# Performance work log

Measured on AMD Instinct MI355X. Metric: run time of the kernel, lower is better.

## Reference

```python
import jax, jax.numpy as jnp
import numpy as np

EMBED_DIM = 1024
B, T = 8, 2048


def setup_inputs() -> dict:
    key = jax.random.key(0)
    kx, kw, kb = jax.random.split(key, 3)
    x = jax.random.normal(kx, (B, T, EMBED_DIM), dtype=jnp.float32)
    # nn.Linear(embed_dim, 3*embed_dim): weight [3E, E], bias [3E]
    bound = 1.0 / np.sqrt(EMBED_DIM)
    W = jax.random.uniform(kw, (3 * EMBED_DIM, EMBED_DIM), minval=-bound, maxval=bound, dtype=jnp.float32)
    b = jax.random.uniform(kb, (3 * EMBED_DIM,), minval=-bound, maxval=bound, dtype=jnp.float32)
    return {"x": x, "W": W, "b": b}


def reference(x, W, b):
    E = x.shape[-1]
    qkv = jnp.einsum('bte,fe->btf', x, W) + b            # [B,T,3E]
    q, k, v = jnp.split(qkv, 3, axis=-1)                 # each [B,T,E]
    scale = 1.0 / jnp.sqrt(jnp.asarray(E, dtype=x.dtype))
    scores = jnp.einsum('bqe,bke->bqk', q, k) * scale    # [B,T,T]
    Tq = x.shape[1]
    causal = jnp.tril(jnp.ones((Tq, Tq), dtype=bool))
    scores = jnp.where(causal[None, :, :], scores, jnp.asarray(-jnp.inf, dtype=x.dtype))
    attn = jax.nn.softmax(scores, axis=-1)
    y = jnp.einsum('bqk,bke->bqe', attn, v)              # [B,T,E]
    return y
```

## Files before the change

### kernel.cpp

```cpp
#include <hip/hip_runtime.h>

typedef unsigned short u16;
typedef unsigned int u32;
typedef __attribute__((ext_vector_type(4))) float f32x4;
typedef __attribute__((ext_vector_type(8))) short bf16x8;

#define T_DIM 2048
#define E_DIM 1024
#define NBATCH 8
#define BK 32
#define BUFP 24576
#define COREP_LDS (3 * BUFP)

struct alignas(8)  U16x4 { u16 x, y, z, w; };
struct alignas(16) F32x4 { float x, y, z, w; };

__device__ __forceinline__ u16 f2bf(float f) {
  u32 u = __float_as_uint(f);
  u += 0x7FFFu + ((u >> 16) & 1u);
  return (u16)(u >> 16);
}

__device__ __forceinline__ void gld16(u16* lds, const u16* g) {
  __builtin_amdgcn_global_load_lds((const __attribute__((address_space(1))) void*)g,
                                   (__attribute__((address_space(3))) void*)lds, 16, 0, 0);
}

__device__ __forceinline__ u32 swz7(u32 x) { return x ^ (((x >> 7) & 7u) << 4); }

__device__ __forceinline__ int xcd_swz(int orig, int nwg) {
  int q = nwg >> 3, r = nwg & 7;
  int x = orig & 7, l = orig >> 3;
  return (x < r ? x * (q + 1) : r * (q + 1) + (x - r) * q) + l;
}

#define LGKM0_PIN() do { asm volatile("s_waitcnt lgkmcnt(0)" ::: "memory"); \
                         __builtin_amdgcn_sched_barrier(0); } while (0)

__device__ __forceinline__ void gemm128n(const u16* __restrict__ A, const u16* __restrict__ B,
                                         int lda, int ldb, int nK, char* lds0, f32x4 acc[4][4])
{
  const int tid = threadIdx.x, lane = tid & 63, wave = tid >> 6;
  const int wr = wave >> 2, wc = wave & 3;

  const u16* sA0; const u16* sBp[2];
  {
    u32 g = swz7((u32)tid * 16u);
    sA0 = A + (size_t)(g >> 6) * lda + ((g & 63u) >> 1);
  }
#pragma unroll
  for (int c = 0; c < 2; ++c) {
    u32 g = swz7((u32)(c * 8192 + tid * 16));
    sBp[c] = B + (size_t)(g >> 6) * ldb + ((g & 63u) >> 1);
  }
  const u32 doff = (u32)tid * 16u;

  auto stageA = [&](char* buf, int t) {
    gld16((u16*)(buf + doff), sA0 + t * BK);
  };
  auto stageB = [&](char* buf, int t) {
#pragma unroll
    for (int c = 0; c < 2; ++c)
      gld16((u16*)(buf + 8192 + c * 8192 + doff), sBp[c] + t * BK);
  };

  const u32 cb = (u32)(lane >> 4) * 16u;
  u32 aoff[4], boff[4];
#pragma unroll
  for (int m = 0; m < 4; ++m)
    aoff[m] = swz7((u32)(wr * 64 + m * 16 + (lane & 15)) * 64u + cb);
#pragma unroll
  for (int n = 0; n < 4; ++n)
    boff[n] = 8192u + swz7((u32)(wc * 64 + n * 16 + (lane & 15)) * 64u + cb);

  stageA(lds0, 0); stageB(lds0, 0);
  stageA(lds0 + BUFP, 1); stageB(lds0 + BUFP, 1);

  int bc = 0;
  bf16x8 a[2], b[4];
  for (int t = 0; t < nK; ++t) {
    char* bufR = lds0 + bc * BUFP;
    int b2 = bc + 2; if (b2 >= 3) b2 -= 3;
    char* bufW = lds0 + b2 * BUFP;

    if (t + 1 < nK) asm volatile("s_waitcnt vmcnt(3)" ::: "memory");
    else            asm volatile("s_waitcnt vmcnt(0)" ::: "memory");
    __builtin_amdgcn_s_barrier();
    __builtin_amdgcn_sched_barrier(0);

    if (t + 2 < nK) stageA(bufW, t + 2);
    a[0] = *(const bf16x8*)(bufR + aoff[0]);
    a[1] = *(const bf16x8*)(bufR + aoff[1]);
#pragma unroll
    for (int n = 0; n < 4; ++n) b[n] = *(const bf16x8*)(bufR + boff[n]);
    LGKM0_PIN();
    __builtin_amdgcn_s_setprio(1);
#pragma unroll
    for (int j = 0; j < 2; ++j)
#pragma unroll
      for (int n = 0; n < 4; ++n)
        acc[j][n] = __builtin_amdgcn_mfma_f32_16x16x32_bf16(a[j], b[n], acc[j][n], 0, 0, 0);
    __builtin_amdgcn_s_setprio(0);
    __builtin_amdgcn_sched_barrier(0);

    if (t + 2 < nK) stageB(bufW, t + 2);
    a[0] = *(const bf16x8*)(bufR + aoff[2]);
    a[1] = *(const bf16x8*)(bufR + aoff[3]);
    LGKM0_PIN();
    __builtin_amdgcn_s_setprio(1);
#pragma unroll
    for (int j = 0; j < 2; ++j)
#pragma unroll
      for (int n = 0; n < 4; ++n)
        acc[2 + j][n] = __builtin_amdgcn_mfma_f32_16x16x32_bf16(a[j], b[n], acc[2 + j][n], 0, 0, 0);
    __builtin_amdgcn_s_setprio(0);
    __builtin_amdgcn_sched_barrier(0);

    bc = bc + 1 == 3 ? 0 : bc + 1;
  }
}

__global__ __launch_bounds__(256) void k_cvt(const float* __restrict__ in, u16* __restrict__ out, int n4)
{
  int i = blockIdx.x * 256 + threadIdx.x;
  if (i >= n4) return;
  F32x4 v = *(const F32x4*)&in[(size_t)i * 4];
  U16x4 o;
  o.x = f2bf(v.x); o.y = f2bf(v.y); o.z = f2bf(v.z); o.w = f2bf(v.w);
  *(U16x4*)&out[(size_t)i * 4] = o;
}

__global__ __launch_bounds__(512, 4) void k_qkv(const u16* __restrict__ Xb, const u16* __restrict__ Wb,
                                                const float* __restrict__ bias,
                                                u16* __restrict__ Q, u16* __restrict__ Kmat,
                                                u16* __restrict__ Vt)
{
  __shared__ __align__(16) char lds[COREP_LDS];
  const int wg = xcd_swz(blockIdx.x, gridDim.x);
  const int my = wg / 12, nx = wg % 12;
  const int m0 = my * 128, n0 = nx * 256;
  const int tid = threadIdx.x, lane = tid & 63, wave = tid >> 6;
  const int wr = wave >> 2, wc = wave & 3;
  f32x4 acc[4][4] = {};
  gemm128n(Xb + (size_t)m0 * E_DIM, Wb + (size_t)n0 * E_DIM, E_DIM, E_DIM, E_DIM / BK, lds, acc);
  __syncthreads();

  char* wsl = lds + wave * 8192;
  const int region = nx >> 2;
  const int nlb = (n0 & (E_DIM - 1)) + wc * 64;
  const int g4 = (lane >> 4) << 2;

  if (region < 2) {
    u16* dst = region ? Kmat : Q;
#pragma unroll
    for (int n = 0; n < 4; ++n) {
      const float bn = bias[n0 + wc * 64 + n * 16 + (lane & 15)];
#pragma unroll
      for (int m = 0; m < 4; ++m)
#pragma unroll
        for (int r = 0; r < 4; ++r) {
          const int rl = m * 16 + g4 + r;
          const int cl = n * 16 + (lane & 15);
          u32 byte = (u32)(rl * 128 + cl * 2) ^ (u32)((rl & 7) << 4);
          *(u16*)(wsl + byte) = f2bf(acc[m][n][r] + bn);
        }
    }
    asm volatile("s_waitcnt lgkmcnt(0)" ::: "memory");
    const int rowb = m0 + wr * 64;
#pragma unroll
    for (int it = 0; it < 8; ++it) {
      const int rl = it * 8 + (lane >> 3);
      const int c16 = lane & 7;
      u32 byte = (u32)(rl * 128 + c16 * 16) ^ (u32)((rl & 7) << 4);
      bf16x8 v = *(const bf16x8*)(wsl + byte);
      *(bf16x8*)&dst[(size_t)(rowb + rl) * E_DIM + nlb + c16 * 8] = v;
    }
  } else {
    const int bl = m0 >> 11;
    const int tb = (m0 & (T_DIM - 1)) + wr * 64;
#pragma unroll
    for (int n = 0; n < 4; ++n) {
      const float bn = bias[n0 + wc * 64 + n * 16 + (lane & 15)];
      const int e_l = n * 16 + (lane & 15);
#pragma unroll
      for (int m = 0; m < 4; ++m)
#pragma unroll
        for (int r = 0; r < 4; ++r) {
          const int tl = m * 16 + g4 + r;
          u32 byte = (u32)(e_l * 128 + tl * 2) ^ (u32)((e_l & 7) << 4);
          *(u16*)(wsl + byte) = f2bf(acc[m][n][r] + bn);
        }
    }
    asm volatile("s_waitcnt lgkmcnt(0)" ::: "memory");
#pragma unroll
    for (int it = 0; it < 8; ++it) {
      const int e_l = it * 8 + (lane >> 3);
      const int t16 = lane & 7;
      u32 byte = (u32)(e_l * 128 + t16 * 16) ^ (u32)((e_l & 7) << 4);
      bf16x8 v = *(const bf16x8*)(wsl + byte);
      *(bf16x8*)&Vt[((size_t)bl * E_DIM + nlb + e_l) * T_DIM + tb + t16 * 8] = v;
    }
  }
}

__global__ __launch_bounds__(512, 4) void k_sp(const u16* __restrict__ Q, const u16* __restrict__ Kmat,
                                               u16* __restrict__ P, float* __restrict__ lc)
{
  __shared__ __align__(16) char lds[COREP_LDS];
  const int wg = xcd_swz(blockIdx.x, gridDim.x);
  const int b = wg / 72;
  int ti = wg % 72;
  int iq = 0;
  while (ti >= (iq >> 1) + 1) { ti -= (iq >> 1) + 1; ++iq; }
  const int ik = ti;
  const int tid = threadIdx.x, lane = tid & 63, wave = tid >> 6;
  const int wr = wave >> 2, wc = wave & 3;
  const int g4 = (lane >> 4) << 2;
  f32x4 acc[4][4] = {};
  const u16* Qp = Q    + (size_t)b * T_DIM * E_DIM + (size_t)iq * 128 * E_DIM;
  const u16* Kp = Kmat + (size_t)b * T_DIM * E_DIM + (size_t)ik * 256 * E_DIM;
  gemm128n(Qp, Kp, E_DIM, E_DIM, E_DIM / BK, lds, acc);
  __syncthreads();

  const float scale = 0.03125f;
  const bool diag = (ik == (iq >> 1));
  const int diagoff = iq * 128 - ik * 256;
#pragma unroll
  for (int n = 0; n < 4; ++n) {
    const int cl = wc * 64 + n * 16 + (lane & 15);
#pragma unroll
    for (int m = 0; m < 4; ++m) {
      const int rl0 = wr * 64 + m * 16 + g4;
#pragma unroll
      for (int r = 0; r < 4; ++r) {
        if (diag && cl > diagoff + rl0 + r) acc[m][n][r] = 0.f;
        else acc[m][n][r] = __expf(fminf(acc[m][n][r] * scale, 60.f));
      }
    }
  }

  float* red2 = (float*)lds;
  float Ls[4][4];
#pragma unroll
  for (int m = 0; m < 4; ++m)
#pragma unroll
    for (int r = 0; r < 4; ++r) {
      float s = acc[m][0][r] + acc[m][1][r] + acc[m][2][r] + acc[m][3][r];
#pragma unroll
      for (int off = 1; off <= 8; off <<= 1) s += __shfl_xor(s, off, 64);
      Ls[m][r] = s;
    }
  if ((lane & 15) == 0) {
#pragma unroll
    for (int m = 0; m < 4; ++m)
#pragma unroll
      for (int r = 0; r < 4; ++r)
        red2[wc * 128 + wr * 64 + m * 16 + g4 + r] = Ls[m][r];
  }
  __syncthreads();
  if (wc == 0 && (lane & 15) == 0) {
#pragma unroll
    for (int m = 0; m < 4; ++m)
#pragma unroll
      for (int r = 0; r < 4; ++r) {
        const int row = wr * 64 + m * 16 + g4 + r;
        const float l = red2[row] + red2[128 + row] + red2[256 + row] + red2[384 + row];
        lc[((size_t)b * T_DIM + iq * 128 + row) * 8 + ik] = l;
      }
  }
  __syncthreads();

  u16* Pb = P + (size_t)b * T_DIM * T_DIM;
  char* wsl = lds + wave * 8192;
#pragma unroll
  for (int n = 0; n < 4; ++n)
#pragma unroll
    for (int m = 0; m < 4; ++m)
#pragma unroll
      for (int r = 0; r < 4; ++r) {
        const int rl = m * 16 + g4 + r;
        const int cl = n * 16 + (lane & 15);
        u32 byte = (u32)(rl * 128 + cl * 2) ^ (u32)((rl & 7) << 4);
        *(u16*)(wsl + byte) = f2bf(acc[m][n][r]);
      }
  asm volatile("s_waitcnt lgkmcnt(0)" ::: "memory");
  const int rowb = iq * 128 + wr * 64;
  const int colb = ik * 256 + wc * 64;
#pragma unroll
  for (int it = 0; it < 8; ++it) {
    const int rl = it * 8 + (lane >> 3);
    const int c16 = lane & 7;
    u32 byte = (u32)(rl * 128 + c16 * 16) ^ (u32)((rl & 7) << 4);
    bf16x8 v = *(const bf16x8*)(wsl + byte);
    *(bf16x8*)&Pb[(size_t)(rowb + rl) * T_DIM + colb + c16 * 8] = v;
  }
}

__global__ __launch_bounds__(256) void k_finish(const float* __restrict__ lc, float* __restrict__ fin)
{
  const int rg = blockIdx.x * 256 + threadIdx.x;
  const int q = rg & (T_DIM - 1);
  const int C = (q >> 8) + 1;
  const float* l = lc + (size_t)rg * 8;
  float L = 0.f;
  for (int c = 0; c < C; ++c) L += l[c];
  fin[rg] = 1.f / L;
}

__global__ __launch_bounds__(512, 2) void k_pv(const u16* __restrict__ P, const u16* __restrict__ Vt,
                                               const float* __restrict__ fin,
                                               float* __restrict__ out, int batch0)
{
  __shared__ __align__(16) char lds[COREP_LDS];
  const int wg = xcd_swz(blockIdx.x, gridDim.x);
  const int bl = wg >> 5, rr = wg & 31;
  const int pr = rr >> 2, ie = rr & 3;
  const int tid = threadIdx.x, lane = tid & 63, wave = tid >> 6;
  const int wr = wave >> 2, wc = wave & 3;

  const u16* Bp = Vt + (size_t)bl * E_DIM * T_DIM + (size_t)ie * 256 * T_DIM;

#pragma unroll
  for (int mem = 0; mem < 2; ++mem) {
    const int iq = mem ? 15 - pr : pr;
    const int nch = (iq >> 1) + 1;

    __syncthreads();
    f32x4 acc[4][4] = {};
    const u16* Ap = P + (size_t)bl * T_DIM * T_DIM + (size_t)iq * 128 * T_DIM;
    gemm128n(Ap, Bp, T_DIM, T_DIM, nch * 8, lds, acc);

#pragma unroll
    for (int m = 0; m < 4; ++m) {
      const int qg0 = iq * 128 + wr * 64 + m * 16 + ((lane >> 4) << 2);
#pragma unroll
      for (int r = 0; r < 4; ++r) {
        const int qg = qg0 + r;
        const float il = fin[bl * T_DIM + qg];
        float* orow = out + ((size_t)(batch0 + bl) * T_DIM + qg) * E_DIM;
#pragma unroll
        for (int n = 0; n < 4; ++n) {
          const int eg = ie * 256 + wc * 64 + n * 16 + (lane & 15);
          orow[eg] = acc[m][n][r] * il;
        }
      }
    }
  }
}

extern "C" void kernel_launch(void* const* d_in, const int* in_sizes, int n_in,
                              void* d_out, int out_size, void* d_ws, size_t ws_size,
                              hipStream_t stream)
{
  const float* x    = (const float*)d_in[0];
  const float* W    = (const float*)d_in[1];
  const float* bias = (const float*)d_in[2];
  float* out = (float*)d_out;

  char* ws = (char*)d_ws;
  const size_t ALIGN = 256;
  auto up = [&](size_t v) { return (v + ALIGN - 1) & ~(ALIGN - 1); };

  const size_t szWb = up((size_t)3 * E_DIM * E_DIM * 2);
  const size_t szX  = up((size_t)T_DIM * E_DIM * 2);
  const size_t szP  = up((size_t)T_DIM * T_DIM * 2);
  const size_t szM  = up((size_t)T_DIM * 8 * 4);
  const size_t szI  = up((size_t)T_DIM * 4);
  const size_t perB = 4 * szX + szP + szM + szI;

  int nb = 1;
  for (int cand = NBATCH; cand >= 1; --cand) {
    if (szWb + (size_t)cand * perB <= ws_size) { nb = cand; break; }
  }

  u16* Wb = (u16*)ws;
  {
    int n4 = 3 * E_DIM * E_DIM / 4;
    k_cvt<<<(n4 + 255) / 256, 256, 0, stream>>>(W, Wb, n4);
  }

  for (int b0 = 0; b0 < NBATCH; b0 += nb) {
    const int nbc = (NBATCH - b0 < nb) ? (NBATCH - b0) : nb;
    size_t o = szWb;
    u16* Xb    = (u16*)(ws + o);   o += (size_t)nbc * szX;
    u16* Qb    = (u16*)(ws + o);   o += (size_t)nbc * szX;
    u16* Kb    = (u16*)(ws + o);   o += (size_t)nbc * szX;
    u16* Vt    = (u16*)(ws + o);   o += (size_t)nbc * szX;
    u16* P     = (u16*)(ws + o);   o += (size_t)nbc * szP;
    float* lcA = (float*)(ws + o); o += (size_t)nbc * szM;
    float* fin = (float*)(ws + o); o += (size_t)nbc * szI;

    {
      int n4 = nbc * T_DIM * E_DIM / 4;
      k_cvt<<<(n4 + 255) / 256, 256, 0, stream>>>(x + (size_t)b0 * T_DIM * E_DIM, Xb, n4);
    }
    k_qkv<<<dim3(192 * nbc), 512, 0, stream>>>(Xb, Wb, bias, Qb, Kb, Vt);
    k_sp<<<dim3(72 * nbc), 512, 0, stream>>>(Qb, Kb, P, lcA);
    k_finish<<<dim3(nbc * T_DIM / 256), 256, 0, stream>>>(lcA, fin);
    k_pv<<<dim3(32 * nbc), 512, 0, stream>>>(P, Vt, fin, out, b0);
  }
}
```

Baseline: 237.9 us.

## Use 128x128 score tiles in QK^T kernel to skip masked causal work

Replaces the 128x256 score tiling in the QK^T/softmax-numerator kernel with 128x128 tiles backed by a new GEMM helper, so causal skipping happens at finer granularity and fewer fully masked blocks are computed. The grid grows from 72 to 136 tiles per batch, the per-row partial-sum buffer widens to 16 chunks, and the finish kernel sums over 128-wide chunks. The P writeback now goes through a block-wide LDS stage using coalesced 16-byte stores. k_pv's launch bounds also change to request higher occupancy. Smaller tiles reduce data reuse per block and may raise register pressure in k_pv.

```diff
diff --git a/kernel.cpp b/kernel.cpp
--- a/kernel.cpp
+++ b/kernel.cpp
@@ -11,6 +11,8 @@
 #define BK 32
 #define BUFP 24576
 #define COREP_LDS (3 * BUFP)
+#define BUFS 16384
+#define CORES_LDS (3 * BUFS)
 
 struct alignas(8)  U16x4 { u16 x, y, z, w; };
 struct alignas(16) F32x4 { float x, y, z, w; };
@@ -112,6 +114,80 @@
     for (int j = 0; j < 2; ++j)
 #pragma unroll
       for (int n = 0; n < 4; ++n)
+        acc[2 + j][n] = __builtin_amdgcn_mfma_f32_16x16x32_bf16(a[j], b[n], acc[2 + j][n], 0, 0, 0);
+    __builtin_amdgcn_s_setprio(0);
+    __builtin_amdgcn_sched_barrier(0);
+
+    bc = bc + 1 == 3 ? 0 : bc + 1;
+  }
+}
+
+__device__ __forceinline__ void gemm128s(const u16* __restrict__ A, const u16* __restrict__ B,
+                                         int lda, int ldb, int nK, char* lds0, f32x4 acc[4][2])
+{
+  const int tid = threadIdx.x, lane = tid & 63, wave = tid >> 6;
+  const int wr = wave >> 2, wc = wave & 3;
+
+  const u16 *sA0, *sB0;
+  {
+    u32 g = swz7((u32)tid * 16u);
+    sA0 = A + (size_t)(g >> 6) * lda + ((g & 63u) >> 1);
+    sB0 = B + (size_t)(g >> 6) * ldb + ((g & 63u) >> 1);
+  }
+  const u32 doff = (u32)tid * 16u;
+
+  auto stage = [&](char* buf, int t) {
+    gld16((u16*)(buf + doff), sA0 + t * BK);
+    gld16((u16*)(buf + 8192 + doff), sB0 + t * BK);
+  };
+
+  const u32 cb = (u32)(lane >> 4) * 16u;
+  u32 aoff[4], boff[2];
+#pragma unroll
+  for (int m = 0; m < 4; ++m)
+    aoff[m] = swz7((u32)(wr * 64 + m * 16 + (lane & 15)) * 64u + cb);
+#pragma unroll
+  for (int n = 0; n < 2; ++n)
+    boff[n] = 8192u + swz7((u32)(wc * 32 + n * 16 + (lane & 15)) * 64u + cb);
+
+  stage(lds0, 0);
+  stage(lds0 + BUFS, 1);
+
+  int bc = 0;
+  bf16x8 a[2], b[2];
+  for (int t = 0; t < nK; ++t) {
+    char* bufR = lds0 + bc * BUFS;
+    int b2 = bc + 2; if (b2 >= 3) b2 -= 3;
+    char* bufW = lds0 + b2 * BUFS;
+
+    if (t + 1 < nK) asm volatile("s_waitcnt vmcnt(2)" ::: "memory");
+    else            asm volatile("s_waitcnt vmcnt(0)" ::: "memory");
+    __builtin_amdgcn_s_barrier();
+    __builtin_amdgcn_sched_barrier(0);
+
+    if (t + 2 < nK) stage(bufW, t + 2);
+    a[0] = *(const bf16x8*)(bufR + aoff[0]);
+    a[1] = *(const bf16x8*)(bufR + aoff[1]);
+    b[0] = *(const bf16x8*)(bufR + boff[0]);
+    b[1] = *(const bf16x8*)(bufR + boff[1]);
+    LGKM0_PIN();
+    __builtin_amdgcn_s_setprio(1);
+#pragma unroll
+    for (int j = 0; j < 2; ++j)
+#pragma unroll
+      for (int n = 0; n < 2; ++n)
+        acc[j][n] = __builtin_amdgcn_mfma_f32_16x16x32_bf16(a[j], b[n], acc[j][n], 0, 0, 0);
+    __builtin_amdgcn_s_setprio(0);
+    __builtin_amdgcn_sched_barrier(0);
+
+    a[0] = *(const bf16x8*)(bufR + aoff[2]);
+    a[1] = *(const bf16x8*)(bufR + aoff[3]);
+    LGKM0_PIN();
+    __builtin_amdgcn_s_setprio(1);
+#pragma unroll
+    for (int j = 0; j < 2; ++j)
+#pragma unroll
+      for (int n = 0; n < 2; ++n)
         acc[2 + j][n] = __builtin_amdgcn_mfma_f32_16x16x32_bf16(a[j], b[n], acc[2 + j][n], 0, 0, 0);
     __builtin_amdgcn_s_setprio(0);
     __builtin_amdgcn_sched_barrier(0);
@@ -206,34 +282,33 @@
 __global__ __launch_bounds__(512, 4) void k_sp(const u16* __restrict__ Q, const u16* __restrict__ Kmat,
                                                u16* __restrict__ P, float* __restrict__ lc)
 {
-  __shared__ __align__(16) char lds[COREP_LDS];
+  __shared__ __align__(16) char lds[CORES_LDS];
   const int wg = xcd_swz(blockIdx.x, gridDim.x);
-  const int b = wg / 72;
-  int ti = wg % 72;
+  const int b = wg / 136;
+  const int ti = wg % 136;
   int iq = 0;
-  while (ti >= (iq >> 1) + 1) { ti -= (iq >> 1) + 1; ++iq; }
-  const int ik = ti;
+  while ((iq + 1) * (iq + 2) / 2 <= ti) ++iq;
+  const int ik = ti - iq * (iq + 1) / 2;
   const int tid = threadIdx.x, lane = tid & 63, wave = tid >> 6;
   const int wr = wave >> 2, wc = wave & 3;
   const int g4 = (lane >> 4) << 2;
-  f32x4 acc[4][4] = {};
+  f32x4 acc[4][2] = {};
   const u16* Qp = Q    + (size_t)b * T_DIM * E_DIM + (size_t)iq * 128 * E_DIM;
-  const u16* Kp = Kmat + (size_t)b * T_DIM * E_DIM + (size_t)ik * 256 * E_DIM;
-  gemm128n(Qp, Kp, E_DIM, E_DIM, E_DIM / BK, lds, acc);
+  const u16* Kp = Kmat + (size_t)b * T_DIM * E_DIM + (size_t)ik * 128 * E_DIM;
+  gemm128s(Qp, Kp, E_DIM, E_DIM, E_DIM / BK, lds, acc);
   __syncthreads();
 
   const float scale = 0.03125f;
-  const bool diag = (ik == (iq >> 1));
-  const int diagoff = iq * 128 - ik * 256;
-#pragma unroll
-  for (int n = 0; n < 4; ++n) {
-    const int cl = wc * 64 + n * 16 + (lane & 15);
+  const bool diag = (ik == iq);
+#pragma unroll
+  for (int n = 0; n < 2; ++n) {
+    const int cl = wc * 32 + n * 16 + (lane & 15);
 #pragma unroll
     for (int m = 0; m < 4; ++m) {
       const int rl0 = wr * 64 + m * 16 + g4;
 #pragma unroll
       for (int r = 0; r < 4; ++r) {
-        if (diag && cl > diagoff + rl0 + r) acc[m][n][r] = 0.f;
+        if (diag && cl > rl0 + r) acc[m][n][r] = 0.f;
         else acc[m][n][r] = __expf(fminf(acc[m][n][r] * scale, 60.f));
       }
     }
@@ -245,7 +320,7 @@
   for (int m = 0; m < 4; ++m)
 #pragma unroll
     for (int r = 0; r < 4; ++r) {
-      float s = acc[m][0][r] + acc[m][1][r] + acc[m][2][r] + acc[m][3][r];
+      float s = acc[m][0][r] + acc[m][1][r];
 #pragma unroll
       for (int off = 1; off <= 8; off <<= 1) s += __shfl_xor(s, off, 64);
       Ls[m][r] = s;
@@ -265,34 +340,33 @@
       for (int r = 0; r < 4; ++r) {
         const int row = wr * 64 + m * 16 + g4 + r;
         const float l = red2[row] + red2[128 + row] + red2[256 + row] + red2[384 + row];
-        lc[((size_t)b * T_DIM + iq * 128 + row) * 8 + ik] = l;
+        lc[((size_t)b * T_DIM + iq * 128 + row) * 16 + ik] = l;
       }
   }
   __syncthreads();
 
   u16* Pb = P + (size_t)b * T_DIM * T_DIM;
-  char* wsl = lds + wave * 8192;
-#pragma unroll
-  for (int n = 0; n < 4; ++n)
+#pragma unroll
+  for (int n = 0; n < 2; ++n)
 #pragma unroll
     for (int m = 0; m < 4; ++m)
 #pragma unroll
       for (int r = 0; r < 4; ++r) {
-        const int rl = m * 16 + g4 + r;
-        const int cl = n * 16 + (lane & 15);
-        u32 byte = (u32)(rl * 128 + cl * 2) ^ (u32)((rl & 7) << 4);
-        *(u16*)(wsl + byte) = f2bf(acc[m][n][r]);
+        const int rl = wr * 64 + m * 16 + g4 + r;
+        const int cl = wc * 32 + n * 16 + (lane & 15);
+        u32 byte = (u32)(rl * 256) + (((u32)(cl * 2)) ^ (u32)((rl & 7) << 4));
+        *(u16*)(lds + byte) = f2bf(acc[m][n][r]);
       }
-  asm volatile("s_waitcnt lgkmcnt(0)" ::: "memory");
-  const int rowb = iq * 128 + wr * 64;
-  const int colb = ik * 256 + wc * 64;
-#pragma unroll
-  for (int it = 0; it < 8; ++it) {
-    const int rl = it * 8 + (lane >> 3);
-    const int c16 = lane & 7;
-    u32 byte = (u32)(rl * 128 + c16 * 16) ^ (u32)((rl & 7) << 4);
-    bf16x8 v = *(const bf16x8*)(wsl + byte);
-    *(bf16x8*)&Pb[(size_t)(rowb + rl) * T_DIM + colb + c16 * 8] = v;
+  __syncthreads();
+  const int rowb = iq * 128;
+  const int colb = ik * 128;
+#pragma unroll
+  for (int it = 0; it < 4; ++it) {
+    const int c = it * 512 + tid;
+    const int rl = c >> 4, cs = c & 15;
+    u32 byte = (u32)(rl * 256) + (((u32)(cs * 16)) ^ (u32)((rl & 7) << 4));
+    bf16x8 v = *(const bf16x8*)(lds + byte);
+    *(bf16x8*)&Pb[(size_t)(rowb + rl) * T_DIM + colb + cs * 8] = v;
   }
 }
 
@@ -300,14 +374,14 @@
 {
   const int rg = blockIdx.x * 256 + threadIdx.x;
   const int q = rg & (T_DIM - 1);
-  const int C = (q >> 8) + 1;
-  const float* l = lc + (size_t)rg * 8;
+  const int C = (q >> 7) + 1;
+  const float* l = lc + (size_t)rg * 16;
   float L = 0.f;
   for (int c = 0; c < C; ++c) L += l[c];
   fin[rg] = 1.f / L;
 }
 
-__global__ __launch_bounds__(512, 2) void k_pv(const u16* __restrict__ P, const u16* __restrict__ Vt,
+__global__ __launch_bounds__(512, 4) void k_pv(const u16* __restrict__ P, const u16* __restrict__ Vt,
                                                const float* __restrict__ fin,
                                                float* __restrict__ out, int batch0)
 {
@@ -364,7 +438,7 @@
   const size_t szWb = up((size_t)3 * E_DIM * E_DIM * 2);
   const size_t szX  = up((size_t)T_DIM * E_DIM * 2);
   const size_t szP  = up((size_t)T_DIM * T_DIM * 2);
-  const size_t szM  = up((size_t)T_DIM * 8 * 4);
+  const size_t szM  = up((size_t)T_DIM * 16 * 4);
   const size_t szI  = up((size_t)T_DIM * 4);
   const size_t perB = 4 * szX + szP + szM + szI;
 
@@ -395,7 +469,7 @@
       k_cvt<<<(n4 + 255) / 256, 256, 0, stream>>>(x + (size_t)b0 * T_DIM * E_DIM, Xb, n4);
     }
     k_qkv<<<dim3(192 * nbc), 512, 0, stream>>>(Xb, Wb, bias, Qb, Kb, Vt);
-    k_sp<<<dim3(72 * nbc), 512, 0, stream>>>(Qb, Kb, P, lcA);
+    k_sp<<<dim3(136 * nbc), 512, 0, stream>>>(Qb, Kb, P, lcA);
     k_finish<<<dim3(nbc * T_DIM / 256), 256, 0, stream>>>(lcA, fin);
     k_pv<<<dim3(32 * nbc), 512, 0, stream>>>(P, Vt, fin, out, b0);
   }
```

Result: slower. 243.5 us (+2.4%).

## Fuse fp32-to-bf16 conversion of x into QKV GEMM A-tile loading

Applied to the files above, without the earlier changes.

Removes the separate k_cvt pass over x. The QKV GEMM now loads fp32 x tiles into registers, converts them to bf16 and writes them into LDS through a register-staged pipeline, while B still uses direct global-to-LDS loads. This avoids writing and re-reading a bf16 copy of x, but the A operand is now read as fp32, doubling its bytes and adding conversion ALU work inside each GEMM tile. The k_pv launch bound is also raised to 4 waves-per-EU occupancy, which may constrain registers.

```diff
diff --git a/kernel.cpp b/kernel.cpp
--- a/kernel.cpp
+++ b/kernel.cpp
@@ -3,6 +3,7 @@
 typedef unsigned short u16;
 typedef unsigned int u32;
 typedef __attribute__((ext_vector_type(4))) float f32x4;
+typedef __attribute__((ext_vector_type(4))) u32 u32x4;
 typedef __attribute__((ext_vector_type(8))) short bf16x8;
 
 #define T_DIM 2048
@@ -120,6 +121,113 @@
   }
 }
 
+__device__ __forceinline__ void gemm128f(const float* __restrict__ Af, const u16* __restrict__ B,
+                                         int lda, int ldb, int nK, char* lds0, f32x4 acc[4][4])
+{
+  const int tid = threadIdx.x, lane = tid & 63, wave = tid >> 6;
+  const int wr = wave >> 2, wc = wave & 3;
+
+  const float* fA;
+  {
+    u32 g = swz7((u32)tid * 16u);
+    fA = Af + (size_t)(g >> 6) * lda + ((g & 63u) >> 1);
+  }
+  const u16* sBp[2];
+#pragma unroll
+  for (int c = 0; c < 2; ++c) {
+    u32 g = swz7((u32)(c * 8192 + tid * 16));
+    sBp[c] = B + (size_t)(g >> 6) * ldb + ((g & 63u) >> 1);
+  }
+  const u32 doff = (u32)tid * 16u;
+
+  auto gldB = [&](char* buf, int t) {
+#pragma unroll
+    for (int c = 0; c < 2; ++c)
+      gld16((u16*)(buf + 8192 + c * 8192 + doff), sBp[c] + t * BK);
+  };
+
+  F32x4 ra, rb;
+  auto loadA = [&](int t) {
+    const float* p = fA + t * BK;
+    ra = *(const F32x4*)p;
+    rb = *(const F32x4*)(p + 4);
+  };
+  auto writeA = [&](char* buf) {
+    u32x4 w;
+    w.x = (u32)f2bf(ra.x) | ((u32)f2bf(ra.y) << 16);
+    w.y = (u32)f2bf(ra.z) | ((u32)f2bf(ra.w) << 16);
+    w.z = (u32)f2bf(rb.x) | ((u32)f2bf(rb.y) << 16);
+    w.w = (u32)f2bf(rb.z) | ((u32)f2bf(rb.w) << 16);
+    *(u32x4*)(buf + doff) = w;
+  };
+
+  const u32 cb = (u32)(lane >> 4) * 16u;
+  u32 aoff[4], boff[4];
+#pragma unroll
+  for (int m = 0; m < 4; ++m)
+    aoff[m] = swz7((u32)(wr * 64 + m * 16 + (lane & 15)) * 64u + cb);
+#pragma unroll
+  for (int n = 0; n < 4; ++n)
+    boff[n] = 8192u + swz7((u32)(wc * 64 + n * 16 + (lane & 15)) * 64u + cb);
+
+  loadA(0);
+  gldB(lds0, 0);
+  asm volatile("s_waitcnt vmcnt(2)" ::: "memory");
+  writeA(lds0);
+  loadA(1);
+  gldB(lds0 + BUFP, 1);
+  asm volatile("s_waitcnt vmcnt(4) lgkmcnt(0)" ::: "memory");
+
+  int bc = 0;
+  bf16x8 a[2], b[4];
+  for (int t = 0; t < nK; ++t) {
+    char* bufR = lds0 + bc * BUFP;
+    int b1 = bc + 1; if (b1 >= 3) b1 -= 3;
+    int b2 = bc + 2; if (b2 >= 3) b2 -= 3;
+
+    __builtin_amdgcn_s_barrier();
+    __builtin_amdgcn_sched_barrier(0);
+
+    if (t + 1 < nK) {
+      asm volatile("s_waitcnt vmcnt(2)" ::: "memory");
+      writeA(lds0 + b1 * BUFP);
+    }
+    if (t + 2 < nK) { loadA(t + 2); gldB(lds0 + b2 * BUFP, t + 2); }
+
+    a[0] = *(const bf16x8*)(bufR + aoff[0]);
+    a[1] = *(const bf16x8*)(bufR + aoff[1]);
+#pragma unroll
+    for (int n = 0; n < 4; ++n) b[n] = *(const bf16x8*)(bufR + boff[n]);
+    LGKM0_PIN();
+    __builtin_amdgcn_s_setprio(1);
+#pragma unroll
+    for (int j = 0; j < 2; ++j)
+#pragma unroll
+      for (int n = 0; n < 4; ++n)
+        acc[j][n] = __builtin_amdgcn_mfma_f32_16x16x32_bf16(a[j], b[n], acc[j][n], 0, 0, 0);
+    __builtin_amdgcn_s_setprio(0);
+    __builtin_amdgcn_sched_barrier(0);
+
+    a[0] = *(const bf16x8*)(bufR + aoff[2]);
+    a[1] = *(const bf16x8*)(bufR + aoff[3]);
+    LGKM0_PIN();
+    __builtin_amdgcn_s_setprio(1);
+#pragma unroll
+    for (int j = 0; j < 2; ++j)
+#pragma unroll
+      for (int n = 0; n < 4; ++n)
+        acc[2 + j][n] = __builtin_amdgcn_mfma_f32_16x16x32_bf16(a[j], b[n], acc[2 + j][n], 0, 0, 0);
+    __builtin_amdgcn_s_setprio(0);
+    __builtin_amdgcn_sched_barrier(0);
+
+    if (t + 1 < nK) {
+      if (t + 2 < nK) asm volatile("s_waitcnt vmcnt(4)" ::: "memory");
+      else            asm volatile("s_waitcnt vmcnt(0)" ::: "memory");
+    }
+    bc = bc + 1 == 3 ? 0 : bc + 1;
+  }
+}
+
 __global__ __launch_bounds__(256) void k_cvt(const float* __restrict__ in, u16* __restrict__ out, int n4)
 {
   int i = blockIdx.x * 256 + threadIdx.x;
@@ -130,7 +238,7 @@
   *(U16x4*)&out[(size_t)i * 4] = o;
 }
 
-__global__ __launch_bounds__(512, 4) void k_qkv(const u16* __restrict__ Xb, const u16* __restrict__ Wb,
+__global__ __launch_bounds__(512, 4) void k_qkv(const float* __restrict__ x, const u16* __restrict__ Wb,
                                                 const float* __restrict__ bias,
                                                 u16* __restrict__ Q, u16* __restrict__ Kmat,
                                                 u16* __restrict__ Vt)
@@ -142,7 +250,7 @@
   const int tid = threadIdx.x, lane = tid & 63, wave = tid >> 6;
   const int wr = wave >> 2, wc = wave & 3;
   f32x4 acc[4][4] = {};
-  gemm128n(Xb + (size_t)m0 * E_DIM, Wb + (size_t)n0 * E_DIM, E_DIM, E_DIM, E_DIM / BK, lds, acc);
+  gemm128f(x + (size_t)m0 * E_DIM, Wb + (size_t)n0 * E_DIM, E_DIM, E_DIM, E_DIM / BK, lds, acc);
   __syncthreads();
 
   char* wsl = lds + wave * 8192;
@@ -307,7 +415,7 @@
   fin[rg] = 1.f / L;
 }
 
-__global__ __launch_bounds__(512, 2) void k_pv(const u16* __restrict__ P, const u16* __restrict__ Vt,
+__global__ __launch_bounds__(512, 4) void k_pv(const u16* __restrict__ P, const u16* __restrict__ Vt,
                                                const float* __restrict__ fin,
                                                float* __restrict__ out, int batch0)
 {
@@ -366,7 +474,7 @@
   const size_t szP  = up((size_t)T_DIM * T_DIM * 2);
   const size_t szM  = up((size_t)T_DIM * 8 * 4);
   const size_t szI  = up((size_t)T_DIM * 4);
-  const size_t perB = 4 * szX + szP + szM + szI;
+  const size_t perB = 3 * szX + szP + szM + szI;
 
   int nb = 1;
   for (int cand = NBATCH; cand >= 1; --cand) {
@@ -382,7 +490,6 @@
   for (int b0 = 0; b0 < NBATCH; b0 += nb) {
     const int nbc = (NBATCH - b0 < nb) ? (NBATCH - b0) : nb;
     size_t o = szWb;
-    u16* Xb    = (u16*)(ws + o);   o += (size_t)nbc * szX;
     u16* Qb    = (u16*)(ws + o);   o += (size_t)nbc * szX;
     u16* Kb    = (u16*)(ws + o);   o += (size_t)nbc * szX;
     u16* Vt    = (u16*)(ws + o);   o += (size_t)nbc * szX;
@@ -390,11 +497,8 @@
     float* lcA = (float*)(ws + o); o += (size_t)nbc * szM;
     float* fin = (float*)(ws + o); o += (size_t)nbc * szI;
 
-    {
-      int n4 = nbc * T_DIM * E_DIM / 4;
-      k_cvt<<<(n4 + 255) / 256, 256, 0, stream>>>(x + (size_t)b0 * T_DIM * E_DIM, Xb, n4);
-    }
-    k_qkv<<<dim3(192 * nbc), 512, 0, stream>>>(Xb, Wb, bias, Qb, Kb, Vt);
+    k_qkv<<<dim3(192 * nbc), 512, 0, stream>>>(x + (size_t)b0 * T_DIM * E_DIM, Wb, bias,
+                                               Qb, Kb, Vt);
     k_sp<<<dim3(72 * nbc), 512, 0, stream>>>(Qb, Kb, P, lcA);
     k_finish<<<dim3(nbc * T_DIM / 256), 256, 0, stream>>>(lcA, fin);
     k_pv<<<dim3(32 * nbc), 512, 0, stream>>>(P, Vt, fin, out, b0);
```

Result: slower. 248.8 us (+4.6%).
